# Performance work log

Hardware: AMD Instinct MI355X
Metric: run time of the kernel (lower is better)

The kernel has to match this reference:

```python
import jax, jax.numpy as jnp
import numpy as np

IOU_THRESH = 0.5
NEG_POS_RATIO = 3
VAR0, VAR1 = 0.1, 0.2  # BoxCoder variances


def box_iou(a, b):
    # a: [G,4] xyxy, b: [P,4] xyxy -> [G,P]
    lt = jnp.maximum(a[:, None, :2], b[None, :, :2])
    rb = jnp.minimum(a[:, None, 2:], b[None, :, 2:])
    wh = jnp.clip(rb - lt, 0.0)
    inter = wh[..., 0] * wh[..., 1]
    area_a = (a[:, 2] - a[:, 0]) * (a[:, 3] - a[:, 1])
    area_b = (b[:, 2] - b[:, 0]) * (b[:, 3] - b[:, 1])
    return inter / (area_a[:, None] + area_b[None, :] - inter)


def xywha_to_xyxy(p):
    c, wh = p[:, :2], p[:, 2:]
    return jnp.concatenate([c - wh * 0.5, c + wh * 0.5], axis=-1)


def assign_targets(gt_boxes, gt_labels, priors_xyxy):
    # gt_boxes [G,4], gt_labels [G], priors_xyxy [P,4]
    iou = box_iou(gt_boxes, priors_xyxy)            # [G,P]
    matched_vals = iou.max(axis=0)                  # [P]
    matches = iou.argmax(axis=0)                    # [P]
    best_prior = iou.argmax(axis=1)                 # [G] best prior per target
    G = gt_boxes.shape[0]
    matches = matches.at[best_prior].set(jnp.arange(G))
    matched_vals = matched_vals.at[best_prior].set(2.0)
    labels = jnp.where(matched_vals < IOU_THRESH, 0, gt_labels[matches])  # [P]
    boxes = gt_boxes[matches]                       # [P,4]
    return boxes, labels


def encode(boxes_xyxy, priors_xywha):
    # SSD center-form encoding with variances
    ctr = (boxes_xyxy[:, :2] + boxes_xyxy[:, 2:]) * 0.5
    wh = boxes_xyxy[:, 2:] - boxes_xyxy[:, :2]
    g_c = (ctr - priors_xywha[:, :2]) / (VAR0 * priors_xywha[:, 2:])
    g_wh = jnp.log(wh / priors_xywha[:, 2:]) / VAR1
    return jnp.concatenate([g_c, g_wh], axis=-1)


def hard_negative_mask(bg_loss, labels):
    # bg_loss [B,P]: -log_softmax(logits)[...,0]; keep all positives and
    # top-(ratio*num_pos) hardest negatives per image.
    pos = labels > 0
    num_neg = pos.sum(axis=1, keepdims=True) * NEG_POS_RATIO
    loss = jnp.where(pos, -jnp.inf, bg_loss)
    order = jnp.argsort(-loss, axis=1)
    rank = jnp.argsort(order, axis=1)
    return pos | (rank < num_neg)


def reference(priors, class_logits, box_regression, gt_boxes, gt_labels):
    priors_xyxy = xywha_to_xyxy(priors)
    boxes, labels = jax.vmap(assign_targets, in_axes=(0, 0, None))(
        gt_boxes, gt_labels, priors_xyxy)            # [B,P,4], [B,P]
    regression_targets = jax.vmap(encode, in_axes=(0, None))(boxes, priors)

    logp = jax.nn.log_softmax(class_logits, axis=-1)  # [B,P,C]
    bg_loss = jax.lax.stop_gradient(-logp[..., 0])
    mask = hard_negative_mask(bg_loss, labels)        # [B,P] bool

    # masked cross-entropy, reduction='sum'
    ce = -jnp.take_along_axis(logp, labels[..., None], axis=-1)[..., 0]
    loss_classifier = jnp.sum(jnp.where(mask, ce, 0.0))

    # masked smooth-L1 (beta=1), reduction='sum' over positives
    pos = labels > 0
    d = jnp.abs(box_regression - regression_targets)
    sl1 = jnp.where(d < 1.0, 0.5 * d * d, d - 0.5)
    loss_box_reg = jnp.sum(jnp.where(pos[..., None], sl1, 0.0))

    num_pos = jnp.sum(pos).astype(class_logits.dtype)
    return loss_box_reg / num_pos, loss_classifier / num_pos


def setup_inputs() -> dict:
    key = jax.random.key(0)
    ks = jax.random.split(key, 8)
    B, P, C, G = 64, 8732, 81, 16
    # priors: xywha in [0,1] with small positive wh
    p_c = jax.random.uniform(ks[0], (P, 2), jnp.float32, 0.05, 0.95)
    p_wh = jax.random.uniform(ks[1], (P, 2), jnp.float32, 0.02, 0.25)
    priors = jnp.concatenate([p_c, p_wh], axis=-1)
    class_logits = jax.random.normal(ks[2], (B, P, C), jnp.float32)
    box_regression = jax.random.normal(ks[3], (B, P, 4), jnp.float32)
    # gt boxes: valid xyxy in [0,1] with positive size
    g_c = jax.random.uniform(ks[4], (B, G, 2), jnp.float32, 0.2, 0.8)
    g_wh = jax.random.uniform(ks[5], (B, G, 2), jnp.float32, 0.05, 0.3)
    gt_boxes = jnp.concatenate([g_c - g_wh * 0.5, g_c + g_wh * 0.5], axis=-1)
    gt_labels = jax.random.randint(ks[6], (B, G), 1, C, jnp.int32)
    return {"priors": priors, "class_logits": class_logits,
            "box_regression": box_regression, "gt_boxes": gt_boxes,
            "gt_labels": gt_labels}
```

## Files before the change

### kernel.cpp

```cpp
#include <hip/hip_runtime.h>
#include <cfloat>

#define GT 16
#define NCLS 81
#define TPB 256
#define BPT 1024
#define MAXP 8732
#define TROWS 64
#define WF4 324
#define TF4 (TROWS*NCLS/4)

__device__ __forceinline__ float smoothl1(float d){
  float a = fabsf(d);
  return a < 1.0f ? 0.5f*a*a : a - 0.5f;
}

__global__ __launch_bounds__(BPT) void bestprior(
    const float* __restrict__ priors,
    const float* __restrict__ gt_boxes,
    int*   __restrict__ best,
    float* __restrict__ ce_pos, float* __restrict__ sl1_sum,
    int* __restrict__ num_pos, float* __restrict__ out, int P)
{
  const int b = blockIdx.x;
  const int tid = threadIdx.x, wave = tid >> 6, lane = tid & 63;
  __shared__ float gx0[GT], gy0[GT], gx1[GT], gy1[GT], ga[GT];
  __shared__ float redv[16*GT]; __shared__ int redi[16*GT];
  if (tid == 0){ ce_pos[b] = 0.0f; sl1_sum[b] = 0.0f; num_pos[b] = 0; }
  if (b == 0 && tid < 2) out[tid] = 0.0f;
  if (tid < GT){
    const float4 gb = ((const float4*)gt_boxes)[b*GT + tid];
    gx0[tid]=gb.x; gy0[tid]=gb.y; gx1[tid]=gb.z; gy1[tid]=gb.w;
    ga[tid] = (gb.z-gb.x)*(gb.w-gb.y);
  }
  __syncthreads();
  float bv[GT]; int bi[GT];
  #pragma unroll
  for (int g=0; g<GT; ++g){ bv[g] = -1.0f; bi[g] = 0x7fffffff; }
  for (int p = tid; p < P; p += BPT){
    const float4 pr = ((const float4*)priors)[p];
    const float px0 = pr.x - pr.z*0.5f, py0 = pr.y - pr.w*0.5f;
    const float px1 = pr.x + pr.z*0.5f, py1 = pr.y + pr.w*0.5f;
    const float pa = (px1-px0)*(py1-py0);
    #pragma unroll
    for (int g=0; g<GT; ++g){
      const float w = fmaxf(fminf(gx1[g],px1) - fmaxf(gx0[g],px0), 0.0f);
      const float h = fmaxf(fminf(gy1[g],py1) - fmaxf(gy0[g],py0), 0.0f);
      const float inter = w*h;
      const float iou = inter / (ga[g] + pa - inter);
      if (iou > bv[g]){ bv[g] = iou; bi[g] = p; }
    }
  }
  #pragma unroll
  for (int g=0; g<GT; ++g){
    float v = bv[g]; int i = bi[g];
    for (int off=32; off>0; off>>=1){
      const float ov = __shfl_down(v, off);
      const int   oi = __shfl_down(i, off);
      if (ov > v || (ov == v && oi < i)){ v = ov; i = oi; }
    }
    if (lane == 0){ redv[wave*GT+g] = v; redi[wave*GT+g] = i; }
  }
  __syncthreads();
  if (tid < GT){
    float v = redv[tid]; int i = redi[tid];
    for (int w=1; w<16; ++w){
      const float ov = redv[w*GT+tid]; const int oi = redi[w*GT+tid];
      if (ov > v || (ov == v && oi < i)){ v = ov; i = oi; }
    }
    best[b*GT + tid] = i;
  }
}

__global__ __launch_bounds__(TPB) void fused_lse(
    const float* __restrict__ priors,
    const float* __restrict__ gt_boxes,
    const int*   __restrict__ gt_labels,
    const float* __restrict__ box_reg,
    const int*   __restrict__ best,
    const float* __restrict__ logits,
    float* __restrict__ bg,
    float* __restrict__ ce_pos,
    float* __restrict__ sl1_sum,
    int*   __restrict__ num_pos,
    int P, int NT)
{
  __shared__ float s[TROWS*NCLS];
  __shared__ float sgx0[2][GT], sgy0[2][GT], sgx1[2][GT], sgy1[2][GT], sga[2][GT];
  __shared__ int   slab[2][GT], sbp[2][GT];
  const int tid = threadIdx.x;
  const int wave = tid >> 6, lane = tid & 63;
  const int rl = lane >> 2, q = lane & 3;
  const int c0 = q ? (1+20*q) : 0;
  const int c1 = 21 + 20*q;
  const int G = gridDim.x;

  const int qn = NT / G, rn = NT % G;
  const int k = blockIdx.x;
  const int t0  = k < rn ? k*(qn+1) : rn*(qn+1) + (k-rn)*qn;
  const int cnt = k < rn ? qn+1 : qn;
  if (cnt <= 0) return;
  const int tend = t0 + cnt;
  const int b0 = (t0*TROWS)/P;
  const int b1 = (tend*TROWS - 1)/P;
  const int boundary = b1*P;

  if (tid < 2*GT){
    const int slot = tid >> 4, g = tid & 15;
    const int bb = slot ? b1 : b0;
    const float4 gb = ((const float4*)gt_boxes)[bb*GT + g];
    sgx0[slot][g]=gb.x; sgy0[slot][g]=gb.y; sgx1[slot][g]=gb.z; sgy1[slot][g]=gb.w;
    sga[slot][g] = (gb.z-gb.x)*(gb.w-gb.y);
    slab[slot][g] = gt_labels[bb*GT + g];
    sbp[slot][g]  = best[bb*GT + g];
  }
  __syncthreads();

  float4 r0,r1,r2,r3,r4,r5, prn, brn;
  auto load_logits = [&](int tt){
    const float4* src = (const float4*)logits + (long long)tt*TF4 + wave*WF4;
    r0 = src[lane]; r1 = src[lane+64]; r2 = src[lane+128];
    r3 = src[lane+192]; r4 = src[lane+256];
    if (lane < 4) r5 = src[lane+320];
  };
  auto load_row = [&](int tt){
    const int rw = tt*TROWS + wave*16 + rl;
    const int bb = (rw >= boundary) ? b1 : b0;
    prn = ((const float4*)priors)[rw - bb*P];
    brn = ((const float4*)box_reg)[rw];
  };
  load_logits(t0); load_row(t0);

  float4* sd = (float4*)(s) + wave*WF4;
  const float* x = s + wave*(WF4*4) + rl*NCLS;
  for (int t = t0; t < tend; ++t){
    sd[lane] = r0; sd[lane+64] = r1; sd[lane+128] = r2;
    sd[lane+192] = r3; sd[lane+256] = r4;
    if (lane < 4) sd[lane+320] = r5;
    const float4 pr = prn, br = brn;
    const int row = t*TROWS + wave*16 + rl;
    const int slot = (row >= boundary);
    const int b = slot ? b1 : b0;
    const int p = row - b*P;
    if (t+1 < tend){ load_logits(t+1); load_row(t+1); }

    const float px0 = pr.x - pr.z*0.5f, py0 = pr.y - pr.w*0.5f;
    const float px1 = pr.x + pr.z*0.5f, py1 = pr.y + pr.w*0.5f;
    const float pa  = (px1-px0)*(py1-py0);
    float mv = -1.0f; int mi = 0;
    const int gbase = q*4;
    #pragma unroll
    for (int j=0; j<4; ++j){
      const int g = gbase + j;
      const float w = fmaxf(fminf(sgx1[slot][g],px1) - fmaxf(sgx0[slot][g],px0), 0.0f);
      const float h = fmaxf(fminf(sgy1[slot][g],py1) - fmaxf(sgy0[slot][g],py0), 0.0f);
      const float inter = w*h;
      const float iou = inter / (sga[slot][g] + pa - inter);
      if (iou > mv){ mv = iou; mi = g; }
    }
    #pragma unroll
    for (int m=1; m<4; m<<=1){
      const float omv = __shfl_xor(mv, m);
      const int   omi = __shfl_xor(mi, m);
      if (omv > mv || (omv == mv && omi < mi)){ mv = omv; mi = omi; }
    }
    int ov = -1;
    #pragma unroll
    for (int j=0; j<4; ++j){
      const int g2 = gbase + j;
      if (sbp[slot][g2] == p) ov = g2;
    }
    #pragma unroll
    for (int m=1; m<4; m<<=1) ov = max(ov, __shfl_xor(ov, m));
    if (ov >= 0){ mv = 2.0f; mi = ov; }

    int lab = 0; float s1 = 0.0f;
    if (q == 0 && mv >= 0.5f){
      lab = slab[slot][mi];
      const float gbx0 = sgx0[slot][mi], gby0 = sgy0[slot][mi];
      const float gbx1 = sgx1[slot][mi], gby1 = sgy1[slot][mi];
      const float ctrx = (gbx0+gbx1)*0.5f, ctry = (gby0+gby1)*0.5f;
      const float wx = gbx1-gbx0, wy = gby1-gby0;
      const float tx = (ctrx - pr.x) / (0.1f*pr.z);
      const float ty = (ctry - pr.y) / (0.1f*pr.w);
      const float tw = __logf(wx/pr.z) / 0.2f;
      const float th = __logf(wy/pr.w) / 0.2f;
      s1 = smoothl1(br.x - tx) + smoothl1(br.y - ty)
         + smoothl1(br.z - tw) + smoothl1(br.w - th);
    }

    float sum = 0.0f;
    for (int c = c0; c < c1; ++c) sum += __expf(x[c]);
    sum += __shfl_xor(sum, 1);
    sum += __shfl_xor(sum, 2);
    if (q == 0){
      const float lse = __logf(sum);
      float bgv;
      if (lab > 0){
        atomicAdd(&ce_pos[b], lse - x[lab]);
        atomicAdd(&sl1_sum[b], s1);
        atomicAdd(&num_pos[b], 1);
        bgv = 0.0f;
      } else {
        bgv = fmaxf(lse - x[0], 0.0f);
      }
      bg[row] = bgv;
    }
  }
}

__global__ __launch_bounds__(TPB) void topk_kernel(
    const float* __restrict__ bg,
    const int*   __restrict__ num_pos,
    const float* __restrict__ sl1_sum,
    const float* __restrict__ ce_pos,
    float* __restrict__ out,
    int P, int B)
{
  const int b = blockIdx.x;
  const int tid = threadIdx.x;
  const int wave = tid >> 6, lane = tid & 63;
  const int rep = tid & 15;
  __shared__ float sv[MAXP];
  __shared__ unsigned cntR[16][257];
  __shared__ unsigned s_wc[4];
  __shared__ float    s_wf[4];
  __shared__ unsigned s_prefix;
  __shared__ int s_krem, s_chosen, s_newk;

  {
    const float4* srcp = (const float4*)(bg + (long long)b * P);
    float4* dst = (float4*)sv;
    for (int j = tid; j < P/4; j += TPB) dst[j] = srcp[j];
  }
  if (tid == 0){
    const int k = 3*num_pos[b];
    s_krem = k < P ? k : P-1;
    s_prefix = 0u;
  }
  __syncthreads();

  for (int level=0; level<4; ++level){
    const int shift = 24 - 8*level;
    for (int i = tid; i < 16*257; i += TPB) ((unsigned*)cntR)[i] = 0u;
    __syncthreads();
    const unsigned pref = s_prefix;
    const int k = s_krem;
    for (int j = tid; j < P/4; j += TPB){
      const float4 f4 = ((const float4*)sv)[j];
      #pragma unroll
      for (int e=0; e<4; ++e){
        const unsigned key = __float_as_uint((&f4.x)[e]);
        const bool ok = (level == 0) || ((key >> (shift+8)) == pref);
        if (ok) atomicAdd(&cntR[rep][(key >> shift) & 255u], 1u);
      }
    }
    __syncthreads();
    const int rb = 255 - tid;
    unsigned c = 0;
    #pragma unroll
    for (int r=0; r<16; ++r) c += cntR[r][rb];
    unsigned cv = c;
    #pragma unroll
    for (int off=1; off<64; off<<=1){
      const unsigned oc = __shfl_up(cv, off);
      if (lane >= off) cv += oc;
    }
    if (lane == 63) s_wc[wave] = cv;
    __syncthreads();
    unsigned addc = 0;
    for (int w=0; w<4; ++w) if (w < wave) addc += s_wc[w];
    const unsigned S = cv - c + addc;
    if ((int)S <= k && k < (int)(S + c)){
      s_chosen = rb; s_newk = k - (int)S;
    }
    __syncthreads();
    if (tid == 0){
      s_krem = s_newk;
      s_prefix = (pref << 8) | (unsigned)s_chosen;
    }
    __syncthreads();
  }
  const unsigned T = s_prefix;
  float acc = 0.0f;
  for (int j = tid; j < P/4; j += TPB){
    const float4 f4 = ((const float4*)sv)[j];
    #pragma unroll
    for (int e=0; e<4; ++e){
      const float f = (&f4.x)[e];
      if (__float_as_uint(f) > T) acc += f;
    }
  }
  for (int off=32; off>0; off>>=1) acc += __shfl_down(acc, off);
  if (lane == 0) s_wf[wave] = acc;
  __syncthreads();
  if (tid < 64){
    float n = 0.0f;
    for (int i = tid; i < B; i += 64) n += (float)num_pos[i];
    for (int off=32; off>0; off>>=1) n += __shfl_down(n, off);
    if (tid == 0){
      const float N = n;
      const float cls = s_wf[0]+s_wf[1]+s_wf[2]+s_wf[3]
                      + (float)s_krem * __uint_as_float(T);
      atomicAdd(&out[0], sl1_sum[b] / N);
      atomicAdd(&out[1], (ce_pos[b] + cls) / N);
    }
  }
}

extern "C" void kernel_launch(void* const* d_in, const int* in_sizes, int n_in,
                              void* d_out, int out_size, void* d_ws, size_t ws_size,
                              hipStream_t stream) {
  const float* priors = (const float*)d_in[0];
  const float* logits = (const float*)d_in[1];
  const float* boxreg = (const float*)d_in[2];
  const float* gtb    = (const float*)d_in[3];
  const int*   gtl    = (const int*)d_in[4];
  const int P = in_sizes[0] / 4;
  const int B = in_sizes[4] / GT;
  const long long BP = (long long)B * P;

  char* ws = (char*)d_ws;
  float* bgv  = (float*)ws;
  int*   best = (int*)(ws + BP*4);
  float* sl1_s= (float*)(ws + BP*4 + 4096);
  int*   npos = (int*)  (ws + BP*4 + 4352);
  float* cep  = (float*)(ws + BP*4 + 4608);

  bestprior<<<B, BPT, 0, stream>>>(priors, gtb, best, cep, sl1_s, npos,
                                   (float*)d_out, P);
  const int NT = (int)(BP / TROWS);
  const int G = 1792;
  fused_lse<<<G, TPB, 0, stream>>>(priors, gtb, gtl, boxreg, best, logits,
                                   bgv, cep, sl1_s, npos, P, NT);
  topk_kernel<<<B, TPB, 0, stream>>>(bgv, npos, sl1_s, cep, (float*)d_out, P, B);
}
```

Baseline: 355.9 us.

## Load logits directly into registers instead of staging through LDS with prefetch

```diff
diff --git a/kernel.cpp b/kernel.cpp
--- a/kernel.cpp
+++ b/kernel.cpp
@@ -7,8 +7,6 @@
 #define BPT 1024
 #define MAXP 8732
 #define TROWS 64
-#define WF4 324
-#define TF4 (TROWS*NCLS/4)
 
 __device__ __forceinline__ float smoothl1(float d){
   float a = fabsf(d);
@@ -85,14 +83,11 @@
     int*   __restrict__ num_pos,
     int P, int NT)
 {
-  __shared__ float s[TROWS*NCLS];
   __shared__ float sgx0[2][GT], sgy0[2][GT], sgx1[2][GT], sgy1[2][GT], sga[2][GT];
   __shared__ int   slab[2][GT], sbp[2][GT];
   const int tid = threadIdx.x;
   const int wave = tid >> 6, lane = tid & 63;
   const int rl = lane >> 2, q = lane & 3;
-  const int c0 = q ? (1+20*q) : 0;
-  const int c1 = 21 + 20*q;
   const int G = gridDim.x;
 
   const int qn = NT / G, rn = NT % G;
@@ -116,33 +111,20 @@
   }
   __syncthreads();
 
-  float4 r0,r1,r2,r3,r4,r5, prn, brn;
-  auto load_logits = [&](int tt){
-    const float4* src = (const float4*)logits + (long long)tt*TF4 + wave*WF4;
-    r0 = src[lane]; r1 = src[lane+64]; r2 = src[lane+128];
-    r3 = src[lane+192]; r4 = src[lane+256];
-    if (lane < 4) r5 = src[lane+320];
-  };
-  auto load_row = [&](int tt){
-    const int rw = tt*TROWS + wave*16 + rl;
-    const int bb = (rw >= boundary) ? b1 : b0;
-    prn = ((const float4*)priors)[rw - bb*P];
-    brn = ((const float4*)box_reg)[rw];
-  };
-  load_logits(t0); load_row(t0);
-
-  float4* sd = (float4*)(s) + wave*WF4;
-  const float* x = s + wave*(WF4*4) + rl*NCLS;
+  const int s = q*20;
   for (int t = t0; t < tend; ++t){
-    sd[lane] = r0; sd[lane+64] = r1; sd[lane+128] = r2;
-    sd[lane+192] = r3; sd[lane+256] = r4;
-    if (lane < 4) sd[lane+320] = r5;
-    const float4 pr = prn, br = brn;
     const int row = t*TROWS + wave*16 + rl;
     const int slot = (row >= boundary);
     const int b = slot ? b1 : b0;
     const int p = row - b*P;
-    if (t+1 < tend){ load_logits(t+1); load_row(t+1); }
+    const float* xr = logits + (long long)row*NCLS;
+
+    float xv[21];
+    #pragma unroll
+    for (int j = 0; j < 21; ++j) xv[j] = xr[s + j];
+
+    const float4 pr = ((const float4*)priors)[p];
+    const float4 br = ((const float4*)box_reg)[row];
 
     const float px0 = pr.x - pr.z*0.5f, py0 = pr.y - pr.w*0.5f;
     const float px1 = pr.x + pr.z*0.5f, py1 = pr.y + pr.w*0.5f;
@@ -189,20 +171,21 @@
          + smoothl1(br.z - tw) + smoothl1(br.w - th);
     }
 
-    float sum = 0.0f;
-    for (int c = c0; c < c1; ++c) sum += __expf(x[c]);
+    float sum = (q == 0) ? __expf(xv[0]) : 0.0f;
+    #pragma unroll
+    for (int j = 1; j < 21; ++j) sum += __expf(xv[j]);
     sum += __shfl_xor(sum, 1);
     sum += __shfl_xor(sum, 2);
     if (q == 0){
       const float lse = __logf(sum);
       float bgv;
       if (lab > 0){
-        atomicAdd(&ce_pos[b], lse - x[lab]);
+        atomicAdd(&ce_pos[b], lse - xr[lab]);
         atomicAdd(&sl1_sum[b], s1);
         atomicAdd(&num_pos[b], 1);
         bgv = 0.0f;
       } else {
-        bgv = fmaxf(lse - x[0], 0.0f);
+        bgv = fmaxf(lse - xv[0], 0.0f);
       }
       bg[row] = bgv;
     }
@@ -330,7 +313,7 @@
   bestprior<<<B, BPT, 0, stream>>>(priors, gtb, best, cep, sl1_s, npos,
                                    (float*)d_out, P);
   const int NT = (int)(BP / TROWS);
-  const int G = 1792;
+  const int G = 2048;
   fused_lse<<<G, TPB, 0, stream>>>(priors, gtb, gtl, boxreg, best, logits,
                                    bgv, cep, sl1_s, npos, P, NT);
   topk_kernel<<<B, TPB, 0, stream>>>(bgv, npos, sl1_s, cep, (float*)d_out, P, B);
```

Result: no change. 354.6 us (-0.4%).
